# Kernel optimization log

Measured on AMD Instinct MI355X. Metric: run time of the kernel, lower is better.

The kernel has to match this reference:

```python
import jax, jax.numpy as jnp
import numpy as np
from jax import lax

B, N, S, K = 8, 8192, 1024, 32
R2 = 0.2 ** 2
EPS = 1e-5


def _gather(p, idx):
    # p: [B, N, C]; idx: [B, ...] int -> p[b, idx[b]]
    bidx = jnp.arange(p.shape[0]).reshape((p.shape[0],) + (1,) * (idx.ndim - 1))
    return p[bidx, idx]


def _fps(xyz):
    # farthest point sampling; deterministic start at index 0 (torch version uses randint)
    def step(carry, _):
        dist, far = carry
        c = _gather(xyz, far[:, None])            # [B,1,3]
        d = jnp.sum((xyz - c) ** 2, -1)           # [B,N]
        dist = jnp.minimum(dist, d)
        return (dist, jnp.argmax(dist, -1).astype(jnp.int32)), far
    init = (jnp.full(xyz.shape[:2], 1e10, xyz.dtype), jnp.zeros((xyz.shape[0],), jnp.int32))
    _, idx = lax.scan(step, init, None, length=S)
    return idx.T                                   # [B,S]


def _ball_query(xyz, new_xyz):
    # squared dists [B,S,N]
    sq = (jnp.sum(new_xyz ** 2, -1)[:, :, None] + jnp.sum(xyz ** 2, -1)[:, None, :]
          - 2.0 * jnp.einsum('bsc,bnc->bsn', new_xyz, xyz))
    gi = jnp.where(sq > R2, N, jnp.arange(N, dtype=jnp.int32))
    # K smallest indices within radius == K largest of (N - gi); equivalent to sort()[:, :, :K]
    vals, _ = lax.top_k(N - gi, K)
    gi = N - vals                                  # [B,S,K]
    first = gi[:, :, :1]
    return jnp.where(gi == N, first, gi)


def _forward(xyz, points, params):
    xyz = xyz.transpose(0, 2, 1)                   # [B,N,3]
    points = points.transpose(0, 2, 1)             # [B,N,C]
    fps_idx = _fps(xyz)                            # [B,S]
    new_xyz = _gather(xyz, fps_idx)                # [B,S,3]
    gi = _ball_query(xyz, new_xyz)                 # [B,S,K]
    g_xyz = _gather(xyz, gi) - new_xyz[:, :, None, :]            # [B,S,K,3]
    g_pts = jnp.concatenate([_gather(points, gi), g_xyz], -1)    # [B,S,K,C+3]
    x = g_pts.transpose(0, 3, 2, 1)                # [B,C+3,K,S]
    for w, b, g, be in params:
        x = jnp.einsum('oc,bcks->boks', w, x) + b[None, :, None, None]
        m = jnp.mean(x, axis=(0, 2, 3), keepdims=True)
        v = jnp.mean((x - m) ** 2, axis=(0, 2, 3), keepdims=True)  # biased var (BN train mode)
        x = jax.nn.relu(g[None, :, None, None] * (x - m) / jnp.sqrt(v + EPS) + be[None, :, None, None])
    return new_xyz.transpose(0, 2, 1), jnp.max(x, axis=2)          # [B,3,S], [B,128,S]


def setup_inputs() -> dict:
    key = jax.random.key(0)
    ks = jax.random.split(key, 8)
    chans = [(67, 64), (64, 64), (64, 128)]
    inp = {
        'xyz': jax.random.normal(ks[0], (B, 3, N), jnp.float32),
        'points': jax.random.normal(ks[1], (B, 64, N), jnp.float32),
    }
    for i, (ci, co) in enumerate(chans):
        kw = jax.random.fold_in(ks[2], i)
        inp[f'w{i}'] = jax.random.normal(kw, (co, ci), jnp.float32) * 0.1
        inp[f'b{i}'] = jnp.zeros((co,), jnp.float32)
        inp[f'g{i}'] = jnp.ones((co,), jnp.float32)
        inp[f'be{i}'] = jnp.zeros((co,), jnp.float32)
    return inp


def reference(xyz, points, w0, b0, g0, be0, w1, b1, g1, be1, w2, b2, g2, be2):
    params = [(w0, b0, g0, be0), (w1, b1, g1, be1), (w2, b2, g2, be2)]
    return _forward(xyz, points, params)
```

## Files before the change

kernel.cpp:

```cpp
#include <hip/hip_runtime.h>

typedef unsigned short ushort_t;
typedef unsigned int uint_t;
typedef unsigned long long u64_t;
typedef unsigned short us8 __attribute__((ext_vector_type(8)));

constexpr int B_ = 8, N_ = 8192, S_ = 1024, K_ = 32;
constexpr int M_ = B_ * S_ * K_;
constexpr float R2_ = 0.04f;
constexpr float EPS_ = 1e-5f;

__device__ __forceinline__ float bf2f(ushort_t u) {
    union { uint_t i; float f; } v; v.i = ((uint_t)u) << 16; return v.f;
}
__device__ __forceinline__ ushort_t f2bf(float f) {
    union { float f; uint_t i; } v; v.f = f;
    uint_t i = v.i;
    uint_t r = (i + 0x7FFFu + ((i >> 16) & 1u)) >> 16;
    return (ushort_t)r;
}

template<int C> __device__ __forceinline__ float dmaxf(float v) {
    int o = __builtin_amdgcn_mov_dpp(__float_as_int(v), C, 0xf, 0xf, true);
    return fmaxf(v, __int_as_float(o));
}

__global__ __launch_bounds__(1024)
void fps_fused(const float* __restrict__ xyz, const float* __restrict__ pts,
               const float* __restrict__ w0, const float* __restrict__ w1,
               const float* __restrict__ w2,
               float* __restrict__ nxyz, float* __restrict__ out0,
               ushort_t* __restrict__ ptT, float* __restrict__ wt,
               float* __restrict__ stats) {
    __shared__ __align__(16) char smem[131072 + 4096 + 64 + 16];
    const int bx = blockIdx.x, t = threadIdx.x;

    if (bx >= 8) {
        if (bx == 264) {
            if (t < 768) stats[t] = 0.0f;
#pragma unroll
            for (int l = 0; l < 3; ++l) {
                const float* w = l == 0 ? w0 : (l == 1 ? w1 : w2);
                int CI = (l == 0) ? 67 : 64;
                int CO = (l == 2) ? 128 : 64;
                float* dst = wt + (l == 0 ? 0 : (l == 1 ? 67 * 64 : 67 * 64 + 64 * 64));
                for (int i = t; i < CI * CO; i += 1024) {
                    int c = i / CO, o = i % CO;
                    dst[c * CO + o] = w[o * CI + c];
                }
            }
            return;
        }
        int g = t >> 8, lt = t & 255;
        int tau = (bx - 8) * 4 + g;
        int b = tau >> 7, n0 = (tau & 127) * 64;
        int tc = lt & 63, tr = lt >> 6;
        ushort_t* tile = (ushort_t*)(smem + g * 8448);
        const float* src = pts + (size_t)b * 64 * N_;
#pragma unroll
        for (int i = 0; i < 16; ++i) {
            int c = i * 4 + tr;
            tile[c * 66 + tc] = f2bf(src[(size_t)c * N_ + n0 + tc]);
        }
        __syncthreads();
#pragma unroll
        for (int i = 0; i < 16; ++i) {
            int nr = i * 4 + tr;
            ptT[((size_t)b * N_ + n0 + nr) * 64 + tc] = tile[tc * 66 + nr];
        }
        return;
    }

    constexpr int T = 1024, P = N_ / T;
    const int b = bx;
    const int lane = t & 63, w = t >> 6;
    const float* X = xyz + (size_t)b * 3 * N_;

    float4* sxyz = (float4*)smem;
    int*    sidx = (int*)(smem + 131072);
    float*  rv   = (float*)(smem + 131072 + 4096);
    int*    sfar = (int*)(smem + 131072 + 4096 + 64);

#pragma unroll
    for (int i = 0; i < P; ++i) {
        int n = t + i * T;
        sxyz[n] = make_float4(X[n], X[N_ + n], X[2 * N_ + n], 0.0f);
    }
    if (t == 0) sidx[0] = 0;
    __syncthreads();

    float px[P], py[P], pz[P], dist[P];
#pragma unroll
    for (int i = 0; i < P; ++i) {
        int j = (i + t) & (P - 1);
        float4 v = sxyz[t * P + j];
        px[j] = v.x; py[j] = v.y; pz[j] = v.z;
        dist[j] = 1e10f;
    }
    float4 cc = sxyz[0];
    float cx = cc.x, cy = cc.y, cz = cc.z;

    for (int s = 0; s < S_; ++s) {
#pragma unroll
        for (int i = 0; i < P; ++i) {
            float dx = __fsub_rn(px[i], cx);
            float dy = __fsub_rn(py[i], cy);
            float dz = __fsub_rn(pz[i], cz);
            float d = __fadd_rn(__fadd_rn(__fmul_rn(dx, dx), __fmul_rn(dy, dy)), __fmul_rn(dz, dz));
            dist[i] = fminf(dist[i], d);
        }
        float a0 = fmaxf(dist[0], dist[4]);
        float a1 = fmaxf(dist[1], dist[5]);
        float a2 = fmaxf(dist[2], dist[6]);
        float a3 = fmaxf(dist[3], dist[7]);
        float lmax = fmaxf(fmaxf(a0, a1), fmaxf(a2, a3));
        float m = lmax;
        m = dmaxf<0x111>(m);
        m = dmaxf<0x112>(m);
        m = dmaxf<0x114>(m);
        m = dmaxf<0x118>(m);
        m = dmaxf<0x142>(m);
        m = dmaxf<0x143>(m);
        if (lane == 63) rv[w] = m;
        __syncthreads();

        float kv0 = rv[lane & 15];
        float kv = kv0;
        kv = dmaxf<0x121>(kv);
        kv = dmaxf<0x122>(kv);
        kv = dmaxf<0x124>(kv);
        kv = dmaxf<0x128>(kv);
        float gmax = kv;
        u64_t wm = __ballot(kv0 == gmax);
        int first_w = __builtin_ctzll(wm);

        if (w == first_w) {
            u64_t lm = __ballot(lmax == gmax);
            int L = __builtin_ctzll(lm);
            if (lane == L) {
                int fi = 0;
#pragma unroll
                for (int i = P - 1; i >= 0; --i)
                    if (dist[i] == gmax) fi = i;
                int nf = t * P + fi;
                *sfar = nf;
                if (s + 1 < S_) sidx[s + 1] = nf;
            }
        }
        __syncthreads();
        int nf = *sfar;
        float4 c = sxyz[nf];
        cx = c.x; cy = c.y; cz = c.z;
    }

    __syncthreads();
    {
        int s = t;
        int idx = sidx[s];
        float4 c = sxyz[idx];
        size_t base = ((size_t)b * S_ + s) * 3;
        nxyz[base + 0] = c.x; nxyz[base + 1] = c.y; nxyz[base + 2] = c.z;
        out0[((size_t)b * 3 + 0) * S_ + s] = c.x;
        out0[((size_t)b * 3 + 1) * S_ + s] = c.y;
        out0[((size_t)b * 3 + 2) * S_ + s] = c.z;
    }
}

__global__ __launch_bounds__(256)
void ballq_kernel(const float* __restrict__ xyz, const float* __restrict__ nxyz,
                  int* __restrict__ gi) {
    int wid = (blockIdx.x * 256 + threadIdx.x) >> 6;
    int lane = threadIdx.x & 63;
    if (wid >= B_ * S_) return;
    int b = wid / S_;
    const float* X = xyz + (size_t)b * 3 * N_;
    float nx = nxyz[(size_t)wid * 3 + 0];
    float ny = nxyz[(size_t)wid * 3 + 1];
    float nz = nxyz[(size_t)wid * 3 + 2];
    float snew = __fadd_rn(__fadd_rn(__fmul_rn(nx, nx), __fmul_rn(ny, ny)), __fmul_rn(nz, nz));
    int cnt = 0; int firstn = 0;
    int* out = gi + (size_t)wid * K_;
    for (int c0 = 0; c0 < N_; c0 += 64) {
        int n = c0 + lane;
        float xx = X[n], xy = X[N_ + n], xz = X[2 * N_ + n];
        float sxn = __fadd_rn(__fadd_rn(__fmul_rn(xx, xx), __fmul_rn(xy, xy)), __fmul_rn(xz, xz));
        float dot = __fadd_rn(__fadd_rn(__fmul_rn(nx, xx), __fmul_rn(ny, xy)), __fmul_rn(nz, xz));
        float sq = __fsub_rn(__fadd_rn(snew, sxn), __fmul_rn(2.0f, dot));
        bool inr = !(sq > R2_);
        unsigned long long mask = __ballot(inr);
        if (cnt == 0 && mask) firstn = c0 + __builtin_ctzll(mask);
        int rank = __popcll(mask & ((1ull << lane) - 1ull));
        if (inr && cnt + rank < K_) out[cnt + rank] = n;
        cnt += (int)__popcll(mask);
        if (cnt >= K_) break;
    }
    if (cnt < K_ && lane >= cnt && lane < K_) out[lane] = firstn;
}

__global__ __launch_bounds__(256)
void layer1_kernel(const ushort_t* __restrict__ ptT,
                   const float* __restrict__ xyz,
                   const float* __restrict__ nxyz,
                   const int* __restrict__ gi,
                   const float* __restrict__ WT,
                   const float* __restrict__ bias,
                   ushort_t* __restrict__ y,
                   float* __restrict__ sums) {
    constexpr int RP = 72;
    __shared__ ushort_t sb[256 * RP];
    __shared__ float ps[128], pq[128];
    int tid = threadIdx.x;
    int m = blockIdx.x * 256 + tid;
    float acc[64];
#pragma unroll
    for (int o = 0; o < 64; ++o) acc[o] = bias[o];

    int idx = gi[m];
    int b = m >> 15;
    const ushort_t* row = ptT + ((size_t)b * N_ + idx) * 64;
#pragma unroll
    for (int c8 = 0; c8 < 8; ++c8) {
        us8 v = *reinterpret_cast<const us8*>(row + c8 * 8);
#pragma unroll
        for (int j = 0; j < 8; ++j) {
            int c = c8 * 8 + j;
            float h = bf2f(v[j]);
            const float* wr = WT + (size_t)c * 64;
#pragma unroll
            for (int o = 0; o < 64; ++o) acc[o] = fmaf(h, wr[o], acc[o]);
        }
    }
    int s = (m >> 5) & (S_ - 1);
    const float* X = xyz + (size_t)b * 3 * N_;
    const float* nx = nxyz + ((size_t)(b * S_ + s)) * 3;
#pragma unroll
    for (int j = 0; j < 3; ++j) {
        float h = X[(size_t)j * N_ + idx] - nx[j];
        const float* wr = WT + (size_t)(64 + j) * 64;
#pragma unroll
        for (int o = 0; o < 64; ++o) acc[o] = fmaf(h, wr[o], acc[o]);
    }
    ushort_t* yr = y + (size_t)m * 64;
#pragma unroll
    for (int v8 = 0; v8 < 8; ++v8) {
        us8 wv;
#pragma unroll
        for (int j = 0; j < 8; ++j) wv[j] = f2bf(acc[v8 * 8 + j]);
        *reinterpret_cast<us8*>(yr + v8 * 8) = wv;
        *reinterpret_cast<us8*>(sb + tid * RP + v8 * 8) = wv;
    }
    __syncthreads();
    if (tid < 128) {
        int c = tid & 63, half = tid >> 6;
        float sv = 0.0f, qv = 0.0f;
        int r0 = half * 128;
        for (int r = 0; r < 128; ++r) {
            float v = bf2f(sb[(r0 + r) * RP + c]);
            sv += v; qv = fmaf(v, v, qv);
        }
        ps[tid] = sv; pq[tid] = qv;
    }
    __syncthreads();
    if (tid < 64) {
        atomicAdd(&sums[tid], ps[tid] + ps[tid + 64]);
        atomicAdd(&sums[128 + tid], pq[tid] + pq[tid + 64]);
    }
}

template<int DO_MAX>
__global__ __launch_bounds__(256, 8)
void layer32_kernel(const ushort_t* __restrict__ xin,
                    const float* __restrict__ WT,
                    const float* __restrict__ bias,
                    const float* __restrict__ sums_in,
                    const float* __restrict__ g,
                    const float* __restrict__ be,
                    ushort_t* __restrict__ y,
                    float* __restrict__ xmax,
                    int COtot,
                    float* __restrict__ sums) {
    constexpr int RP = 40;
    __shared__ ushort_t sb[256 * RP];
    __shared__ float ps[64], pq[64];
    __shared__ float s_a[64], s_sh[64];
    int tid = threadIdx.x;
    if (tid < 64) {
        float mean = sums_in[tid] * (1.0f / (float)M_);
        float var = sums_in[128 + tid] * (1.0f / (float)M_) - mean * mean;
        float a = g[tid] / sqrtf(var + EPS_);
        s_a[tid] = a;
        s_sh[tid] = be[tid] - mean * a;
    }
    __syncthreads();

    int m = blockIdx.x * 256 + tid;
    int os = blockIdx.y * 32;
    float acc[32];
#pragma unroll
    for (int o = 0; o < 32; ++o) acc[o] = bias[os + o];

    const ushort_t* row = xin + (size_t)m * 64;
#pragma unroll
    for (int c8 = 0; c8 < 8; ++c8) {
        us8 v = *reinterpret_cast<const us8*>(row + c8 * 8);
#pragma unroll
        for (int j = 0; j < 8; ++j) {
            int c = c8 * 8 + j;
            float h = fmaxf(fmaf(s_a[c], bf2f(v[j]), s_sh[c]), 0.0f);
            const float* wr = WT + (size_t)c * COtot + os;
#pragma unroll
            for (int o = 0; o < 32; ++o) acc[o] = fmaf(h, wr[o], acc[o]);
        }
    }
#pragma unroll
    for (int v8 = 0; v8 < 4; ++v8) {
        us8 wv;
#pragma unroll
        for (int j = 0; j < 8; ++j) wv[j] = f2bf(acc[v8 * 8 + j]);
        if (!DO_MAX) {
            ushort_t* yr = y + (size_t)m * COtot + os;
            *reinterpret_cast<us8*>(yr + v8 * 8) = wv;
        }
        *reinterpret_cast<us8*>(sb + tid * RP + v8 * 8) = wv;
    }
    __syncthreads();
    if (DO_MAX) {
        int gq = tid >> 5, c = tid & 31;
        float mv = -1e30f;
        int r0 = gq * 32;
#pragma unroll 8
        for (int r = 0; r < 32; ++r) mv = fmaxf(mv, bf2f(sb[(r0 + r) * RP + c]));
        xmax[((size_t)(blockIdx.x * 8 + gq)) * 128 + os + c] = mv;
    }
    if (tid < 64) {
        int c = tid & 31, half = tid >> 5;
        float sv = 0.0f, qv = 0.0f;
        int r0 = half * 128;
        for (int r = 0; r < 128; ++r) {
            float v = bf2f(sb[(r0 + r) * RP + c]);
            sv += v; qv = fmaf(v, v, qv);
        }
        ps[tid] = sv; pq[tid] = qv;
    }
    __syncthreads();
    if (tid < 64) {
        int cg = os + (tid & 31);
        if (tid < 32) {
            atomicAdd(&sums[cg], ps[tid] + ps[tid + 32]);
            atomicAdd(&sums[128 + cg], pq[tid] + pq[tid + 32]);
        }
    }
}

__global__ __launch_bounds__(256)
void final_max(const float* __restrict__ xmax, const float* __restrict__ sums,
               const float* __restrict__ g, const float* __restrict__ be,
               float* __restrict__ out1) {
    __shared__ float s_a[128], s_sh[128];
    int t = threadIdx.x;
    if (t < 128) {
        float mean = sums[t] * (1.0f / (float)M_);
        float var = sums[128 + t] * (1.0f / (float)M_) - mean * mean;
        float a = g[t] / sqrtf(var + EPS_);
        s_a[t] = a;
        s_sh[t] = be[t] - mean * a;
    }
    __syncthreads();
    int gw = blockIdx.x * 4 + (t >> 6);
    if (gw >= B_ * S_) return;
    int lane = t & 63;
    int b = gw / S_, s = gw % S_;
    int c0 = lane * 2;
    float v0 = xmax[(size_t)gw * 128 + c0];
    float v1 = xmax[(size_t)gw * 128 + c0 + 1];
    float f0 = fmaf(v0, s_a[c0], s_sh[c0]);
    float f1 = fmaf(v1, s_a[c0 + 1], s_sh[c0 + 1]);
    out1[((size_t)b * 128 + c0) * S_ + s] = fmaxf(f0, 0.0f);
    out1[((size_t)b * 128 + c0 + 1) * S_ + s] = fmaxf(f1, 0.0f);
}

extern "C" void kernel_launch(void* const* d_in, const int* in_sizes, int n_in,
                              void* d_out, int out_size, void* d_ws, size_t ws_size,
                              hipStream_t stream) {
    const float* xyz = (const float*)d_in[0];
    const float* pts = (const float*)d_in[1];
    const float* w0 = (const float*)d_in[2];
    const float* b0 = (const float*)d_in[3];
    const float* g0 = (const float*)d_in[4];
    const float* be0 = (const float*)d_in[5];
    const float* w1 = (const float*)d_in[6];
    const float* b1 = (const float*)d_in[7];
    const float* g1 = (const float*)d_in[8];
    const float* be1 = (const float*)d_in[9];
    const float* w2 = (const float*)d_in[10];
    const float* b2 = (const float*)d_in[11];
    const float* g2 = (const float*)d_in[12];
    const float* be2 = (const float*)d_in[13];

    float* out0 = (float*)d_out;
    float* out1 = out0 + (size_t)B_ * 3 * S_;

    char* ws = (char*)d_ws;
    float*    nxyz  = (float*)(ws + 32768);
    int*      gi    = (int*)(ws + 131072);
    float*    stats = (float*)(ws + 1179648);
    float*    wt    = (float*)(ws + 1185792);
    ushort_t* ptT   = (ushort_t*)(ws + 2097152);
    ushort_t* xA    = (ushort_t*)(ws + 10485760);
    float*    xmax  = (float*)(ws + 10485760);
    ushort_t* xB    = (ushort_t*)(ws + 77594624);

    fps_fused<<<265, 1024, 0, stream>>>(xyz, pts, w0, w1, w2, nxyz, out0, ptT, wt, stats);
    ballq_kernel<<<(B_ * S_) / 4, 256, 0, stream>>>(xyz, nxyz, gi);

    layer1_kernel<<<M_ / 256, 256, 0, stream>>>(ptT, xyz, nxyz, gi, wt, b0, xA, stats + 0);

    layer32_kernel<0><<<dim3(M_ / 256, 2), 256, 0, stream>>>(
        xA, wt + 67 * 64, b1, stats + 0, g0, be0, xB, nullptr, 64, stats + 256);

    layer32_kernel<1><<<dim3(M_ / 256, 4), 256, 0, stream>>>(
        xB, wt + 67 * 64 + 64 * 64, b2, stats + 256, g1, be1, nullptr, xmax, 128, stats + 512);

    final_max<<<(B_ * S_) / 4, 256, 0, stream>>>(xmax, stats + 512, g2, be2, out1);
}
```

Baseline: 1.188 ms.

## Fuse ball query into layer1 kernel and widen BN stat reductions

Measured after the change: 1.210 ms. About the same (+1.9%).

```diff
diff --git a/kernel.cpp b/kernel.cpp
--- a/kernel.cpp
+++ b/kernel.cpp
@@ -167,56 +167,57 @@
 }
 
 __global__ __launch_bounds__(256)
-void ballq_kernel(const float* __restrict__ xyz, const float* __restrict__ nxyz,
-                  int* __restrict__ gi) {
-    int wid = (blockIdx.x * 256 + threadIdx.x) >> 6;
-    int lane = threadIdx.x & 63;
-    if (wid >= B_ * S_) return;
-    int b = wid / S_;
-    const float* X = xyz + (size_t)b * 3 * N_;
-    float nx = nxyz[(size_t)wid * 3 + 0];
-    float ny = nxyz[(size_t)wid * 3 + 1];
-    float nz = nxyz[(size_t)wid * 3 + 2];
-    float snew = __fadd_rn(__fadd_rn(__fmul_rn(nx, nx), __fmul_rn(ny, ny)), __fmul_rn(nz, nz));
-    int cnt = 0; int firstn = 0;
-    int* out = gi + (size_t)wid * K_;
-    for (int c0 = 0; c0 < N_; c0 += 64) {
-        int n = c0 + lane;
-        float xx = X[n], xy = X[N_ + n], xz = X[2 * N_ + n];
-        float sxn = __fadd_rn(__fadd_rn(__fmul_rn(xx, xx), __fmul_rn(xy, xy)), __fmul_rn(xz, xz));
-        float dot = __fadd_rn(__fadd_rn(__fmul_rn(nx, xx), __fmul_rn(ny, xy)), __fmul_rn(nz, xz));
-        float sq = __fsub_rn(__fadd_rn(snew, sxn), __fmul_rn(2.0f, dot));
-        bool inr = !(sq > R2_);
-        unsigned long long mask = __ballot(inr);
-        if (cnt == 0 && mask) firstn = c0 + __builtin_ctzll(mask);
-        int rank = __popcll(mask & ((1ull << lane) - 1ull));
-        if (inr && cnt + rank < K_) out[cnt + rank] = n;
-        cnt += (int)__popcll(mask);
-        if (cnt >= K_) break;
-    }
-    if (cnt < K_ && lane >= cnt && lane < K_) out[lane] = firstn;
-}
-
-__global__ __launch_bounds__(256)
 void layer1_kernel(const ushort_t* __restrict__ ptT,
                    const float* __restrict__ xyz,
                    const float* __restrict__ nxyz,
-                   const int* __restrict__ gi,
                    const float* __restrict__ WT,
                    const float* __restrict__ bias,
                    ushort_t* __restrict__ y,
                    float* __restrict__ sums) {
     constexpr int RP = 72;
     __shared__ ushort_t sb[256 * RP];
-    __shared__ float ps[128], pq[128];
+    __shared__ float ps[256], pq[256];
+    __shared__ int sgi[8][32];
     int tid = threadIdx.x;
-    int m = blockIdx.x * 256 + tid;
+    const int bx = blockIdx.x;
+    const int wv = tid >> 6, lane = tid & 63;
+    const int b = bx >> 7;
+    const float* X = xyz + (size_t)b * 3 * N_;
+
+#pragma unroll
+    for (int qq = 0; qq < 2; ++qq) {
+        int lq = wv * 2 + qq;
+        int gw = bx * 8 + lq;
+        float nx = nxyz[(size_t)gw * 3 + 0];
+        float ny = nxyz[(size_t)gw * 3 + 1];
+        float nz = nxyz[(size_t)gw * 3 + 2];
+        float snew = __fadd_rn(__fadd_rn(__fmul_rn(nx, nx), __fmul_rn(ny, ny)), __fmul_rn(nz, nz));
+        int cnt = 0; int firstn = 0;
+        int* out = sgi[lq];
+        for (int c0 = 0; c0 < N_; c0 += 64) {
+            int n = c0 + lane;
+            float xx = X[n], xy = X[N_ + n], xz = X[2 * N_ + n];
+            float sxn = __fadd_rn(__fadd_rn(__fmul_rn(xx, xx), __fmul_rn(xy, xy)), __fmul_rn(xz, xz));
+            float dot = __fadd_rn(__fadd_rn(__fmul_rn(nx, xx), __fmul_rn(ny, xy)), __fmul_rn(nz, xz));
+            float sq = __fsub_rn(__fadd_rn(snew, sxn), __fmul_rn(2.0f, dot));
+            bool inr = !(sq > R2_);
+            unsigned long long mask = __ballot(inr);
+            if (cnt == 0 && mask) firstn = c0 + __builtin_ctzll(mask);
+            int rank = __popcll(mask & ((1ull << lane) - 1ull));
+            if (inr && cnt + rank < K_) out[cnt + rank] = n;
+            cnt += (int)__popcll(mask);
+            if (cnt >= K_) break;
+        }
+        if (cnt < K_ && lane >= cnt && lane < K_) out[lane] = firstn;
+    }
+    __syncthreads();
+
+    int m = bx * 256 + tid;
+    int idx = sgi[tid >> 5][tid & 31];
     float acc[64];
 #pragma unroll
     for (int o = 0; o < 64; ++o) acc[o] = bias[o];
 
-    int idx = gi[m];
-    int b = m >> 15;
     const ushort_t* row = ptT + ((size_t)b * N_ + idx) * 64;
 #pragma unroll
     for (int c8 = 0; c8 < 8; ++c8) {
@@ -231,7 +232,6 @@
         }
     }
     int s = (m >> 5) & (S_ - 1);
-    const float* X = xyz + (size_t)b * 3 * N_;
     const float* nx = nxyz + ((size_t)(b * S_ + s)) * 3;
 #pragma unroll
     for (int j = 0; j < 3; ++j) {
@@ -243,18 +243,18 @@
     ushort_t* yr = y + (size_t)m * 64;
 #pragma unroll
     for (int v8 = 0; v8 < 8; ++v8) {
-        us8 wv;
-#pragma unroll
-        for (int j = 0; j < 8; ++j) wv[j] = f2bf(acc[v8 * 8 + j]);
-        *reinterpret_cast<us8*>(yr + v8 * 8) = wv;
-        *reinterpret_cast<us8*>(sb + tid * RP + v8 * 8) = wv;
-    }
-    __syncthreads();
-    if (tid < 128) {
-        int c = tid & 63, half = tid >> 6;
+        us8 wv8;
+#pragma unroll
+        for (int j = 0; j < 8; ++j) wv8[j] = f2bf(acc[v8 * 8 + j]);
+        *reinterpret_cast<us8*>(yr + v8 * 8) = wv8;
+        *reinterpret_cast<us8*>(sb + tid * RP + v8 * 8) = wv8;
+    }
+    __syncthreads();
+    {
+        int c = tid & 63, qd = tid >> 6;
         float sv = 0.0f, qv = 0.0f;
-        int r0 = half * 128;
-        for (int r = 0; r < 128; ++r) {
+        int r0 = qd * 64;
+        for (int r = 0; r < 64; ++r) {
             float v = bf2f(sb[(r0 + r) * RP + c]);
             sv += v; qv = fmaf(v, v, qv);
         }
@@ -262,8 +262,8 @@
     }
     __syncthreads();
     if (tid < 64) {
-        atomicAdd(&sums[tid], ps[tid] + ps[tid + 64]);
-        atomicAdd(&sums[128 + tid], pq[tid] + pq[tid + 64]);
+        atomicAdd(&sums[tid], (ps[tid] + ps[tid + 64]) + (ps[tid + 128] + ps[tid + 192]));
+        atomicAdd(&sums[128 + tid], (pq[tid] + pq[tid + 64]) + (pq[tid + 128] + pq[tid + 192]));
     }
 }
 
@@ -281,7 +281,7 @@
                     float* __restrict__ sums) {
     constexpr int RP = 40;
     __shared__ ushort_t sb[256 * RP];
-    __shared__ float ps[64], pq[64];
+    __shared__ float ps[256], pq[256];
     __shared__ float s_a[64], s_sh[64];
     int tid = threadIdx.x;
     if (tid < 64) {
@@ -332,23 +332,25 @@
         for (int r = 0; r < 32; ++r) mv = fmaxf(mv, bf2f(sb[(r0 + r) * RP + c]));
         xmax[((size_t)(blockIdx.x * 8 + gq)) * 128 + os + c] = mv;
     }
-    if (tid < 64) {
-        int c = tid & 31, half = tid >> 5;
+    {
+        int c = tid & 31, oct = tid >> 5;
         float sv = 0.0f, qv = 0.0f;
-        int r0 = half * 128;
-        for (int r = 0; r < 128; ++r) {
+        int r0 = oct * 32;
+        for (int r = 0; r < 32; ++r) {
             float v = bf2f(sb[(r0 + r) * RP + c]);
             sv += v; qv = fmaf(v, v, qv);
         }
         ps[tid] = sv; pq[tid] = qv;
     }
     __syncthreads();
-    if (tid < 64) {
-        int cg = os + (tid & 31);
-        if (tid < 32) {
-            atomicAdd(&sums[cg], ps[tid] + ps[tid + 32]);
-            atomicAdd(&sums[128 + cg], pq[tid] + pq[tid + 32]);
-        }
+    if (tid < 32) {
+        int cg = os + tid;
+        float s4 = ((ps[tid] + ps[tid + 32]) + (ps[tid + 64] + ps[tid + 96]))
+                 + ((ps[tid + 128] + ps[tid + 160]) + (ps[tid + 192] + ps[tid + 224]));
+        float q4 = ((pq[tid] + pq[tid + 32]) + (pq[tid + 64] + pq[tid + 96]))
+                 + ((pq[tid + 128] + pq[tid + 160]) + (pq[tid + 192] + pq[tid + 224]));
+        atomicAdd(&sums[cg], s4);
+        atomicAdd(&sums[128 + cg], q4);
     }
 }
 
@@ -402,7 +404,6 @@
 
     char* ws = (char*)d_ws;
     float*    nxyz  = (float*)(ws + 32768);
-    int*      gi    = (int*)(ws + 131072);
     float*    stats = (float*)(ws + 1179648);
     float*    wt    = (float*)(ws + 1185792);
     ushort_t* ptT   = (ushort_t*)(ws + 2097152);
@@ -411,9 +412,8 @@
     ushort_t* xB    = (ushort_t*)(ws + 77594624);
 
     fps_fused<<<265, 1024, 0, stream>>>(xyz, pts, w0, w1, w2, nxyz, out0, ptT, wt, stats);
-    ballq_kernel<<<(B_ * S_) / 4, 256, 0, stream>>>(xyz, nxyz, gi);
-
-    layer1_kernel<<<M_ / 256, 256, 0, stream>>>(ptT, xyz, nxyz, gi, wt, b0, xA, stats + 0);
+
+    layer1_kernel<<<M_ / 256, 256, 0, stream>>>(ptT, xyz, nxyz, wt, b0, xA, stats + 0);
 
     layer32_kernel<0><<<dim3(M_ / 256, 2), 256, 0, stream>>>(
         xA, wt + 67 * 64, b1, stats + 0, g0, be0, xB, nullptr, 64, stats + 256);
```
